# Kernel optimization log

Measured on AMD Instinct MI355X. Metric: run time of the kernel, lower is better.

Reference implementation:

```python
import jax, jax.numpy as jnp
import numpy as np

Q_CHAN = 8          # q_chan
IN_CHAN = 128
KS = 56             # kernel_size; ks*ks must equal h*w
STRIDE = 2
BN_EPS = 1e-5


def setup_inputs() -> dict:
    key = jax.random.key(0)
    ks = jax.random.split(key, 10)
    n, c, h, w = 4, IN_CHAN, 56, 56
    hw = h * w  # 3136 == KS*KS
    oc = 4 * Q_CHAN  # qkv conv output channels = 32
    return {
        "x": jax.random.normal(ks[0], (n, c, h, w), dtype=jnp.float32),
        # 1x1 conv weight (out_ch, in_ch) and bias
        "w_qkv": jax.random.normal(ks[1], (oc, c), dtype=jnp.float32) * (1.0 / np.sqrt(c)),
        "b_qkv": jnp.zeros((oc,), dtype=jnp.float32),
        # BatchNorm (inference mode) affine + running stats
        "bn_gamma": jnp.ones((oc,), dtype=jnp.float32),
        "bn_beta": jnp.zeros((oc,), dtype=jnp.float32),
        "bn_mean": jnp.zeros((oc,), dtype=jnp.float32),
        "bn_var": jnp.ones((oc,), dtype=jnp.float32),
        # learned relative position biases, trailing dim = ks*ks = h*w
        "rq": jax.random.normal(ks[2], (Q_CHAN, KS * KS), dtype=jnp.float32),
        "rk": jax.random.normal(ks[3], (Q_CHAN, KS * KS), dtype=jnp.float32),
        "rv": jax.random.normal(ks[4], (2 * Q_CHAN, KS * KS), dtype=jnp.float32),
    }


def reference(x, w_qkv, b_qkv, bn_gamma, bn_beta, bn_mean, bn_var, rq, rk, rv):
    n, c, h, w = x.shape
    # 1x1 conv + inference BatchNorm
    qkv = jnp.einsum('nchw,oc->nohw', x, w_qkv) + b_qkv[None, :, None, None]
    scale = bn_gamma / jnp.sqrt(bn_var + BN_EPS)
    qkv = (qkv - bn_mean[None, :, None, None]) * scale[None, :, None, None] + bn_beta[None, :, None, None]
    qkv = qkv.reshape(n, 4 * Q_CHAN, h * w)
    q = qkv[:, :Q_CHAN]            # [n, 8, hw]
    k = qkv[:, Q_CHAN:2 * Q_CHAN]  # [n, 8, hw]
    v = qkv[:, 2 * Q_CHAN:]        # [n, 16, hw]
    # global attention scores with learned positional bias terms: [n, hw, hw]
    sc = (jnp.einsum('nci,ncj->nij', q, k)
          + jnp.einsum('ci,ncj->nij', rq, q)
          + jnp.einsum('ci,ncj->nij', rk, k))
    sc = jax.nn.softmax(sc, axis=2)
    v = v + rv[None]
    out = jnp.einsum('nij,ncj->nci', sc, v).reshape(n, 2 * Q_CHAN, h, w)
    # AvgPool2d(kernel=stride, stride=stride)
    s = STRIDE
    out = out.reshape(n, 2 * Q_CHAN, h // s, s, w // s, s).mean(axis=(3, 5))
    return out
```

## Files before the change

### kernel.cpp

```cpp
#include <hip/hip_runtime.h>

#define HW 3136
#define CIN 128
#define MHAT 40.0f
#define NSEV 7
#define LOG2E 1.44269504088896340736f
#define NEGC  (-57.7078018f)

typedef __attribute__((ext_vector_type(8))) short bf16x8;
typedef __attribute__((ext_vector_type(4))) float f32x4;

__device__ __forceinline__ short f2bf(float f) {
    union { float f; unsigned u; } v; v.f = f;
    unsigned r = v.u + 0x7fffu + ((v.u >> 16) & 1u);
    return (short)(r >> 16);
}
__device__ __forceinline__ float bf2f(short s) {
    union { unsigned u; float f; } v; v.u = ((unsigned)(unsigned short)s) << 16;
    return v.f;
}
__device__ __forceinline__ unsigned pk(short a, short b) {
    return (unsigned)(unsigned short)a | ((unsigned)(unsigned short)b << 16);
}
__device__ __forceinline__ unsigned cvtpk(float a, float b) {
    unsigned r;
    asm("v_cvt_pk_bf16_f32 %0, %1, %2" : "=v"(r) : "v"(a), "v"(b));
    return r;
}
__device__ __forceinline__ float lo2f(unsigned p) { return __uint_as_float(p << 16); }
__device__ __forceinline__ float hi2f(unsigned p) { return __uint_as_float(p & 0xffff0000u); }
__device__ __forceinline__ float exp2_hw(float x) {
    float r;
    asm("v_exp_f32 %0, %1" : "=v"(r) : "v"(x));
    return r;
}

union UF { bf16x8 v; unsigned u[4]; };


__global__ __launch_bounds__(256) void proj_mfma(
    const float* __restrict__ x, const float* __restrict__ w,
    const float* __restrict__ bq, const float* __restrict__ gm,
    const float* __restrict__ bt, const float* __restrict__ mu,
    const float* __restrict__ vr, const float* __restrict__ rq,
    const float* __restrict__ rk, const float* __restrict__ rv,
    float* __restrict__ WS, float* __restrict__ ASQ)
{
    const int tid = threadIdx.x;
    const int wv = tid >> 6, lane = tid & 63;
    const int il = lane & 15, q = lane >> 4;
    const int jb = blockIdx.x * 64;
    const int nn = blockIdx.y;
    const int z  = blockIdx.z;
    const int jA = jb + wv * 16 + il;
    const float* xn = x + (size_t)nn * CIN * HW;

    UF ah[4], al[4];
    #pragma unroll
    for (int s = 0; s < 4; ++s) {
        float xv[8];
        #pragma unroll
        for (int u = 0; u < 8; ++u)
            xv[u] = xn[(size_t)(s * 32 + q * 8 + u) * HW + jA];
        #pragma unroll
        for (int t = 0; t < 4; ++t) {
            unsigned hp = cvtpk(xv[2 * t], xv[2 * t + 1]);
            unsigned lp = cvtpk(xv[2 * t] - lo2f(hp), xv[2 * t + 1] - hi2f(hp));
            ah[s].u[t] = hp;
            al[s].u[t] = lp;
        }
    }
    UF wh[4], wl[4];
    const float* wp = w + (size_t)(z * 16 + il) * CIN;
    #pragma unroll
    for (int s = 0; s < 4; ++s) {
        float4 f0 = *(const float4*)(wp + s * 32 + q * 8);
        float4 f1 = *(const float4*)(wp + s * 32 + q * 8 + 4);
        float wf[8] = {f0.x, f0.y, f0.z, f0.w, f1.x, f1.y, f1.z, f1.w};
        #pragma unroll
        for (int t = 0; t < 4; ++t) {
            unsigned hp = cvtpk(wf[2 * t], wf[2 * t + 1]);
            unsigned lp = cvtpk(wf[2 * t] - lo2f(hp), wf[2 * t + 1] - hi2f(hp));
            wh[s].u[t] = hp;
            wl[s].u[t] = lp;
        }
    }

    f32x4 d = {0.f, 0.f, 0.f, 0.f};
    #pragma unroll
    for (int s = 0; s < 4; ++s) d = __builtin_amdgcn_mfma_f32_16x16x32_bf16(ah[s].v, wh[s].v, d, 0, 0, 0);
    #pragma unroll
    for (int s = 0; s < 4; ++s) d = __builtin_amdgcn_mfma_f32_16x16x32_bf16(al[s].v, wh[s].v, d, 0, 0, 0);
    #pragma unroll
    for (int s = 0; s < 4; ++s) d = __builtin_amdgcn_mfma_f32_16x16x32_bf16(ah[s].v, wl[s].v, d, 0, 0, 0);

    const int ch = z * 16 + il;
    const float sc = gm[ch] * rsqrtf(vr[ch] + 1e-5f);
    const float sh = (bq[ch] - mu[ch]) * sc + bt[ch];
    #pragma unroll
    for (int r = 0; r < 4; ++r) {
        const int j = jb + wv * 16 + q * 4 + r;
        float val = d[r] * sc + sh;
        const size_t base = (size_t)nn * HW + j;
        if (z == 0) {
            WS[base * 32 + il] = val;
            float a = (il < 8) ? (val + rk[il * HW + j]) : rq[(il - 8) * HW + j];
            ASQ[base * 16 + il] = a * LOG2E;
        } else {
            WS[base * 32 + 16 + il] = val + rv[il * HW + j];
        }
    }
}

#define JT 224
#define QKS 40
#define VTS 232

__global__ __launch_bounds__(256) void attn_mfma(
    const float* __restrict__ WS, const float* __restrict__ ASQ,
    float* __restrict__ ONUM, float* __restrict__ OLS)
{
    __shared__ short QK[JT * QKS];
    __shared__ short VT[16 * VTS];
    __shared__ short PB[4 * 16 * QKS];
    const int tid = threadIdx.x;
    const int wv = tid >> 6, lane = tid & 63;
    const int il = lane & 15, q = lane >> 4;
    const int b   = blockIdx.x;
    const int sev = b % NSEV;
    const int ig  = b / NSEV;
    const int nn  = ig / 49;
    const int i0  = (ig % 49) * 64 + wv * 16;
    const float* wsn = WS + (size_t)nn * HW * 32;

    bf16x8 bco;
    {
        const float* cp = ASQ + ((size_t)nn * HW + i0 + il) * 16 + (q & 1) * 8;
        float4 f0 = *(const float4*)cp;
        float4 f1 = *(const float4*)(cp + 4);
        float cf[8] = {f0.x, f0.y, f0.z, f0.w, f1.x, f1.y, f1.z, f1.w};
        UF bb;
        #pragma unroll
        for (int t = 0; t < 4; ++t) {
            unsigned hp = cvtpk(cf[2 * t], cf[2 * t + 1]);
            unsigned lp = cvtpk(cf[2 * t] - lo2f(hp), cf[2 * t + 1] - hi2f(hp));
            bb.u[t] = (q < 2) ? hp : lp;
        }
        bco = bb.v;
    }

    const bf16x8 zero8 = {0, 0, 0, 0, 0, 0, 0, 0};
    const f32x4 DINIT = {NEGC, NEGC, NEGC, NEGC};
    f32x4 outc = {0.f, 0.f, 0.f, 0.f};
    float lsum = 0.f;
    short* prow = &PB[(wv * 16 + il) * QKS];

    #pragma unroll 1
    for (int ck = 0; ck < 2; ++ck) {
        const int jb = (sev * 2 + ck) * JT;
        __syncthreads();
        if (tid < JT) {
            const float* src = wsn + (size_t)(jb + tid) * 32;
            float4 v0 = *(const float4*)src;
            float4 v1 = *(const float4*)(src + 4);
            float4 v2 = *(const float4*)(src + 8);
            float4 v3 = *(const float4*)(src + 12);
            float g[16] = {v2.x, v2.y, v2.z, v2.w, v3.x, v3.y, v3.z, v3.w,
                           v0.x, v0.y, v0.z, v0.w, v1.x, v1.y, v1.z, v1.w};
            short* row = &QK[tid * QKS];
            #pragma unroll
            for (int t = 0; t < 8; ++t) {
                unsigned hp = cvtpk(g[2 * t], g[2 * t + 1]);
                unsigned lp = cvtpk(g[2 * t] - lo2f(hp), g[2 * t + 1] - hi2f(hp));
                *(unsigned*)&row[2 * t]      = hp;
                *(unsigned*)&row[16 + 2 * t] = lp;
            }
        }
        {
            const int c = tid & 15, jg = tid >> 4;
            const float* vsrc = wsn + (size_t)(jb + jg * 14) * 32 + 16 + c;
            short* vrow = &VT[c * VTS + jg * 14];
            #pragma unroll
            for (int k = 0; k < 7; ++k)
                *(unsigned*)&vrow[2 * k] = cvtpk(vsrc[(2 * k) * 32], vsrc[(2 * k + 1) * 32]);
        }
        __syncthreads();

        #pragma unroll 2
        for (int step = 0; step < 14; ++step) {
            const short* arow = &QK[(step * 16 + il) * QKS + (q & 1) * 8];
            bf16x8 a1 = *(const bf16x8*)arow;
            bf16x8 a2 = *(const bf16x8*)(arow + 16);
            a2 = (lane < 32) ? a2 : zero8;
            f32x4 d = __builtin_amdgcn_mfma_f32_16x16x32_bf16(a1, bco, DINIT, 0, 0, 0);
            d = __builtin_amdgcn_mfma_f32_16x16x32_bf16(a2, bco, d, 0, 0, 0);
            float p0 = exp2_hw(d[0]), p1 = exp2_hw(d[1]);
            float p2 = exp2_hw(d[2]), p3 = exp2_hw(d[3]);
            lsum += (p0 + p1) + (p2 + p3);
            const int pc = (step & 1) * 16 + q * 4;
            *(unsigned*)&prow[pc]     = cvtpk(p0, p1);
            *(unsigned*)&prow[pc + 2] = cvtpk(p2, p3);
            if (step & 1) {
                bf16x8 ap = *(const bf16x8*)&PB[(wv * 16 + il) * QKS + q * 8];
                bf16x8 bv = *(const bf16x8*)&VT[il * VTS + (step >> 1) * 32 + q * 8];
                outc = __builtin_amdgcn_mfma_f32_16x16x32_bf16(ap, bv, outc, 0, 0, 0);
            }
        }
    }

    lsum += __shfl_xor(lsum, 16);
    lsum += __shfl_xor(lsum, 32);
    float* np = ONUM + ((size_t)(sev * 4 + nn) * HW + i0) * 16;
    #pragma unroll
    for (int r = 0; r < 4; ++r)
        np[(q * 4 + r) * 16 + il] = outc[r];
    if (lane < 16)
        OLS[(size_t)(sev * 4 + nn) * HW + i0 + lane] = lsum;
}

__global__ void pool_kernel(const float* __restrict__ ONUM, const float* __restrict__ OLS,
                            float* __restrict__ out) {
    int idx = blockIdx.x * blockDim.x + threadIdx.x;
    if (idx >= 4 * 16 * 28 * 28) return;
    int ow = idx % 28, oh = (idx / 28) % 28;
    int rest = idx / 784;
    int nn = rest >> 4, c = rest & 15;
    float s = 0.f;
    #pragma unroll
    for (int dh = 0; dh < 2; ++dh)
        #pragma unroll
        for (int dw = 0; dw < 2; ++dw) {
            int i = (2 * oh + dh) * 56 + 2 * ow + dw;
            float num = 0.f, l = 0.f;
            #pragma unroll
            for (int p = 0; p < NSEV; ++p) {
                num += ONUM[((size_t)(p * 4 + nn) * HW + i) * 16 + c];
                l   += OLS[(size_t)(p * 4 + nn) * HW + i];
            }
            s += num / l;
        }
    out[idx] = 0.25f * s;
}

#define FJC 392
#define FPSTR 394

__global__ __launch_bounds__(512, 2) void fused_attn(
    const float* __restrict__ x, const float* __restrict__ w,
    const float* __restrict__ bq, const float* __restrict__ gm,
    const float* __restrict__ bt, const float* __restrict__ mu,
    const float* __restrict__ vr, const float* __restrict__ rq,
    const float* __restrict__ rk, const float* __restrict__ rv,
    float* __restrict__ out)
{
    __shared__ float PT[32][FPSTR];
    __shared__ float SQ[56][16];
    __shared__ float ST[56][17];

    const int tid  = threadIdx.x;
    const int wv   = tid >> 6, lane = tid & 63;
    const int bid  = blockIdx.x;
    const int nn   = bid / 56, rem = bid % 56;
    const int oh   = rem >> 1, half = rem & 1;
    const float* xn = x + (size_t)nn * CIN * HW;

    if (tid < 448) {
        int r = tid >> 3, c = tid & 7;
        int rh = (r >= 28) ? 1 : 0, rw = r - 28*rh;
        int i  = (2*oh + rh)*56 + half*28 + rw;
        float acc = 0.f;
        for (int cc = 0; cc < CIN; ++cc)
            acc += xn[cc*HW + i] * w[c*CIN + cc];
        float s  = gm[c] * rsqrtf(vr[c] + 1e-5f);
        float qv = (acc + bq[c] - mu[c])*s + bt[c];
        SQ[r][c]   = qv + rk[c*HW + i];
        SQ[r][8+c] = rq[c*HW + i];
    }

    float l_[7];
    float ac_[7][16];
    #pragma unroll
    for (int r = 0; r < 7; ++r) {
        l_[r] = 0.f;
        #pragma unroll
        for (int c = 0; c < 16; ++c) ac_[r][c] = 0.f;
    }
    __syncthreads();

    for (int cb = 0; cb < 8; ++cb) {
        const int jbase = cb * FJC;
        const int o0 = wv * 4;
        for (int t = 0; t < 4; ++t) {
            int p = lane + 64*t;
            if (p < 196) {
                int j0 = jbase + 2*p;
                float a0x=0.f,a0y=0.f,a1x=0.f,a1y=0.f,a2x=0.f,a2y=0.f,a3x=0.f,a3y=0.f;
                for (int cc = 0; cc < CIN; ++cc) {
                    float2 xv = *(const float2*)(xn + (size_t)cc*HW + j0);
                    float w0 = w[(o0+0)*CIN + cc];
                    float w1 = w[(o0+1)*CIN + cc];
                    float w2 = w[(o0+2)*CIN + cc];
                    float w3 = w[(o0+3)*CIN + cc];
                    a0x += xv.x*w0; a0y += xv.y*w0;
                    a1x += xv.x*w1; a1y += xv.y*w1;
                    a2x += xv.x*w2; a2y += xv.y*w2;
                    a3x += xv.x*w3; a3y += xv.y*w3;
                }
                #pragma unroll
                for (int u = 0; u < 4; ++u) {
                    int o = o0 + u;
                    float av0 = (u==0)? a0x : (u==1)? a1x : (u==2)? a2x : a3x;
                    float av1 = (u==0)? a0y : (u==1)? a1y : (u==2)? a2y : a3y;
                    float s  = gm[o] * rsqrtf(vr[o] + 1e-5f);
                    float sh = (bq[o] - mu[o])*s + bt[o];
                    float v0 = av0*s + sh, v1 = av1*s + sh;
                    if (o >= 16) {
                        v0 += rv[(o-16)*HW + j0];
                        v1 += rv[(o-16)*HW + j0 + 1];
                    }
                    *(float2*)&PT[o][2*p] = make_float2(v0, v1);
                }
            }
        }
        __syncthreads();

        #pragma unroll
        for (int rr = 0; rr < 7; rr += 2) {
            const bool two = (rr + 1) < 7;
            const int ra = wv*7 + rr;
            float A1a[8], A2a[8], A1b[8], A2b[8];
            #pragma unroll
            for (int c = 0; c < 8; ++c) {
                A1a[c] = SQ[ra][c];   A2a[c] = SQ[ra][8+c];
                A1b[c] = two ? SQ[ra+1][c]   : 0.f;
                A2b[c] = two ? SQ[ra+1][8+c] : 0.f;
            }
            for (int t = 0; t < 7; ++t) {
                int jl = 64*t + lane;
                if (jl < FJC) {
                    float qv[8], kv[8], vv[16];
                    #pragma unroll
                    for (int c = 0; c < 8; ++c) { qv[c] = PT[c][jl]; kv[c] = PT[8+c][jl]; }
                    #pragma unroll
                    for (int c = 0; c < 16; ++c) vv[c] = PT[16+c][jl];
                    float sa = 0.f, sb = 0.f;
                    #pragma unroll
                    for (int c = 0; c < 8; ++c) {
                        sa += A1a[c]*kv[c] + A2a[c]*qv[c];
                        sb += A1b[c]*kv[c] + A2b[c]*qv[c];
                    }
                    float pa = __expf(sa - MHAT);
                    l_[rr] += pa;
                    #pragma unroll
                    for (int c = 0; c < 16; ++c) ac_[rr][c] += pa * vv[c];
                    if (two) {
                        float pb = __expf(sb - MHAT);
                        l_[rr+1] += pb;
                        #pragma unroll
                        for (int c = 0; c < 16; ++c) ac_[rr+1][c] += pb * vv[c];
                    }
                }
            }
        }
        __syncthreads();
    }

    #pragma unroll
    for (int rr = 0; rr < 7; ++rr) {
        int r = wv*7 + rr;
        float l = l_[rr];
        #pragma unroll
        for (int off = 32; off; off >>= 1) l += __shfl_xor(l, off);
        if (lane == 0) ST[r][16] = l;
        #pragma unroll
        for (int c = 0; c < 16; ++c) {
            float a = ac_[rr][c];
            #pragma unroll
            for (int off = 32; off; off >>= 1) a += __shfl_xor(a, off);
            if (lane == c) ST[r][c] = a;
        }
    }
    __syncthreads();

    if (tid < 224) {
        int c = tid & 15, qq = tid >> 4;
        float s = 0.f;
        #pragma unroll
        for (int rh = 0; rh < 2; ++rh)
            #pragma unroll
            for (int dw = 0; dw < 2; ++dw) {
                int r = rh*28 + 2*qq + dw;
                s += ST[r][c] / ST[r][16];
            }
        out[((nn*16 + c)*28 + oh)*28 + half*14 + qq] = 0.25f * s;
    }
}

extern "C" void kernel_launch(void* const* d_in, const int* in_sizes, int n_in,
                              void* d_out, int out_size, void* d_ws, size_t ws_size,
                              hipStream_t stream) {
    const float* x     = (const float*)d_in[0];
    const float* w     = (const float*)d_in[1];
    const float* bq    = (const float*)d_in[2];
    const float* gm    = (const float*)d_in[3];
    const float* bt    = (const float*)d_in[4];
    const float* mu    = (const float*)d_in[5];
    const float* vr    = (const float*)d_in[6];
    const float* rq    = (const float*)d_in[7];
    const float* rk    = (const float*)d_in[8];
    const float* rv    = (const float*)d_in[9];
    float* out = (float*)d_out;

    const size_t WSF  = (size_t)4 * HW * 32;
    const size_t ASQF = (size_t)4 * HW * 16;
    const size_t ONF  = (size_t)NSEV * 4 * HW * 16;
    const size_t OLF  = (size_t)NSEV * 4 * HW;
    const size_t NEED = (WSF + ASQF + ONF + OLF) * sizeof(float);

    if (ws_size >= NEED) {
        float* WS   = (float*)d_ws;
        float* ASQ  = WS + WSF;
        float* ONUM = ASQ + ASQF;
        float* OLS  = ONUM + ONF;
        proj_mfma<<<dim3(49, 4, 2), 256, 0, stream>>>(x, w, bq, gm, bt, mu, vr, rq, rk, rv, WS, ASQ);
        attn_mfma<<<dim3(196 * NSEV), 256, 0, stream>>>(WS, ASQ, ONUM, OLS);
        pool_kernel<<<dim3(196), 256, 0, stream>>>(ONUM, OLS, out);
    } else {
        fused_attn<<<dim3(224), dim3(512), 0, stream>>>(x, w, bq, gm, bt, mu, vr, rq, rk, rv, out);
    }
}
```

Baseline: 110.4 us.

## Emit pre-split bf16 hi/lo Q/K and transposed V from projection kernel

The projection kernel now writes Q/K and the per-query coefficient vectors already split into bf16 hi/lo pairs in the exact row layout the attention kernel copies into shared memory, and writes V+rv as bf16 in channel-major order. The attention kernel then does plain vector copies instead of float loads plus per-block bf16 split conversions, which halves global traffic and removes conversion work repeated across the 7 key-chunk blocks. The block index mapping also changes so blocks sharing a key chunk are adjacent. The projection's MFMA operands are swapped for z==0 to get a transposed output layout, and its accumulation is split into two accumulators.

```diff
diff --git a/kernel.cpp b/kernel.cpp
--- a/kernel.cpp
+++ b/kernel.cpp
@@ -10,18 +10,6 @@
 typedef __attribute__((ext_vector_type(8))) short bf16x8;
 typedef __attribute__((ext_vector_type(4))) float f32x4;
 
-__device__ __forceinline__ short f2bf(float f) {
-    union { float f; unsigned u; } v; v.f = f;
-    unsigned r = v.u + 0x7fffu + ((v.u >> 16) & 1u);
-    return (short)(r >> 16);
-}
-__device__ __forceinline__ float bf2f(short s) {
-    union { unsigned u; float f; } v; v.u = ((unsigned)(unsigned short)s) << 16;
-    return v.f;
-}
-__device__ __forceinline__ unsigned pk(short a, short b) {
-    return (unsigned)(unsigned short)a | ((unsigned)(unsigned short)b << 16);
-}
 __device__ __forceinline__ unsigned cvtpk(float a, float b) {
     unsigned r;
     asm("v_cvt_pk_bf16_f32 %0, %1, %2" : "=v"(r) : "v"(a), "v"(b));
@@ -44,7 +32,7 @@
     const float* __restrict__ bt, const float* __restrict__ mu,
     const float* __restrict__ vr, const float* __restrict__ rq,
     const float* __restrict__ rk, const float* __restrict__ rv,
-    float* __restrict__ WS, float* __restrict__ ASQ)
+    short* __restrict__ QKWS, short* __restrict__ ASQB, short* __restrict__ VWS)
 {
     const int tid = threadIdx.x;
     const int wv = tid >> 6, lane = tid & 63;
@@ -55,7 +43,7 @@
     const int jA = jb + wv * 16 + il;
     const float* xn = x + (size_t)nn * CIN * HW;
 
-    UF ah[4], al[4];
+    UF xh[4], xl[4];
     #pragma unroll
     for (int s = 0; s < 4; ++s) {
         float xv[8];
@@ -66,8 +54,8 @@
         for (int t = 0; t < 4; ++t) {
             unsigned hp = cvtpk(xv[2 * t], xv[2 * t + 1]);
             unsigned lp = cvtpk(xv[2 * t] - lo2f(hp), xv[2 * t + 1] - hi2f(hp));
-            ah[s].u[t] = hp;
-            al[s].u[t] = lp;
+            xh[s].u[t] = hp;
+            xl[s].u[t] = lp;
         }
     }
     UF wh[4], wl[4];
@@ -86,29 +74,68 @@
         }
     }
 
-    f32x4 d = {0.f, 0.f, 0.f, 0.f};
-    #pragma unroll
-    for (int s = 0; s < 4; ++s) d = __builtin_amdgcn_mfma_f32_16x16x32_bf16(ah[s].v, wh[s].v, d, 0, 0, 0);
-    #pragma unroll
-    for (int s = 0; s < 4; ++s) d = __builtin_amdgcn_mfma_f32_16x16x32_bf16(al[s].v, wh[s].v, d, 0, 0, 0);
-    #pragma unroll
-    for (int s = 0; s < 4; ++s) d = __builtin_amdgcn_mfma_f32_16x16x32_bf16(ah[s].v, wl[s].v, d, 0, 0, 0);
-
-    const int ch = z * 16 + il;
-    const float sc = gm[ch] * rsqrtf(vr[ch] + 1e-5f);
-    const float sh = (bq[ch] - mu[ch]) * sc + bt[ch];
-    #pragma unroll
-    for (int r = 0; r < 4; ++r) {
-        const int j = jb + wv * 16 + q * 4 + r;
-        float val = d[r] * sc + sh;
-        const size_t base = (size_t)nn * HW + j;
-        if (z == 0) {
-            WS[base * 32 + il] = val;
-            float a = (il < 8) ? (val + rk[il * HW + j]) : rq[(il - 8) * HW + j];
-            ASQ[base * 16 + il] = a * LOG2E;
-        } else {
-            WS[base * 32 + 16 + il] = val + rv[il * HW + j];
-        }
+    f32x4 a0 = {0.f, 0.f, 0.f, 0.f}, a1 = {0.f, 0.f, 0.f, 0.f};
+    if (z == 0) {
+        #pragma unroll
+        for (int s = 0; s < 4; ++s) a0 = __builtin_amdgcn_mfma_f32_16x16x32_bf16(wh[s].v, xh[s].v, a0, 0, 0, 0);
+        #pragma unroll
+        for (int s = 0; s < 4; ++s) a1 = __builtin_amdgcn_mfma_f32_16x16x32_bf16(wl[s].v, xh[s].v, a1, 0, 0, 0);
+        #pragma unroll
+        for (int s = 0; s < 4; ++s) a1 = __builtin_amdgcn_mfma_f32_16x16x32_bf16(wh[s].v, xl[s].v, a1, 0, 0, 0);
+    } else {
+        #pragma unroll
+        for (int s = 0; s < 4; ++s) a0 = __builtin_amdgcn_mfma_f32_16x16x32_bf16(xh[s].v, wh[s].v, a0, 0, 0, 0);
+        #pragma unroll
+        for (int s = 0; s < 4; ++s) a1 = __builtin_amdgcn_mfma_f32_16x16x32_bf16(xl[s].v, wh[s].v, a1, 0, 0, 0);
+        #pragma unroll
+        for (int s = 0; s < 4; ++s) a1 = __builtin_amdgcn_mfma_f32_16x16x32_bf16(xh[s].v, wl[s].v, a1, 0, 0, 0);
+    }
+    const f32x4 d = a0 + a1;
+
+    if (z == 0) {
+        const int jj = jA;
+        float hv[4], av[4];
+        #pragma unroll
+        for (int r = 0; r < 4; ++r) {
+            const int ch = q * 4 + r;
+            const float sc = gm[ch] * rsqrtf(vr[ch] + 1e-5f);
+            const float sh = (bq[ch] - mu[ch]) * sc + bt[ch];
+            const float val = d[r] * sc + sh;
+            hv[r] = val;
+            const float a = (ch < 8) ? (val + rk[(size_t)ch * HW + jj])
+                                     : rq[(size_t)(ch - 8) * HW + jj];
+            av[r] = a * LOG2E;
+        }
+        short* qrow = QKWS + ((size_t)nn * HW + jj) * 32;
+        short* arow = ASQB + ((size_t)nn * HW + jj) * 32;
+        const int pb = (q * 4) ^ 8;
+        unsigned h01 = cvtpk(hv[0], hv[1]), h23 = cvtpk(hv[2], hv[3]);
+        unsigned l01 = cvtpk(hv[0] - lo2f(h01), hv[1] - hi2f(h01));
+        unsigned l23 = cvtpk(hv[2] - lo2f(h23), hv[3] - hi2f(h23));
+        *(unsigned*)&qrow[pb]          = h01;
+        *(unsigned*)&qrow[pb + 2]      = h23;
+        *(unsigned*)&qrow[16 + pb]     = l01;
+        *(unsigned*)&qrow[16 + pb + 2] = l23;
+        unsigned c01 = cvtpk(av[0], av[1]), c23 = cvtpk(av[2], av[3]);
+        unsigned e01 = cvtpk(av[0] - lo2f(c01), av[1] - hi2f(c01));
+        unsigned e23 = cvtpk(av[2] - lo2f(c23), av[3] - hi2f(c23));
+        *(unsigned*)&arow[q * 4]          = c01;
+        *(unsigned*)&arow[q * 4 + 2]      = c23;
+        *(unsigned*)&arow[16 + q * 4]     = e01;
+        *(unsigned*)&arow[16 + q * 4 + 2] = e23;
+    } else {
+        const int ch = 16 + il;
+        const float sc = gm[ch] * rsqrtf(vr[ch] + 1e-5f);
+        const float sh = (bq[ch] - mu[ch]) * sc + bt[ch];
+        const int jbase = jb + wv * 16 + q * 4;
+        float4 rvv = *(const float4*)(rv + (size_t)il * HW + jbase);
+        float v0 = d[0] * sc + sh + rvv.x;
+        float v1 = d[1] * sc + sh + rvv.y;
+        float v2 = d[2] * sc + sh + rvv.z;
+        float v3 = d[3] * sc + sh + rvv.w;
+        short* vp = VWS + (size_t)(nn * 16 + il) * HW + jbase;
+        *(unsigned*)&vp[0] = cvtpk(v0, v1);
+        *(unsigned*)&vp[2] = cvtpk(v2, v3);
     }
 }
 
@@ -117,7 +144,8 @@
 #define VTS 232
 
 __global__ __launch_bounds__(256) void attn_mfma(
-    const float* __restrict__ WS, const float* __restrict__ ASQ,
+    const short* __restrict__ QKWS, const short* __restrict__ ASQB,
+    const short* __restrict__ VWS,
     float* __restrict__ ONUM, float* __restrict__ OLS)
 {
     __shared__ short QK[JT * QKS];
@@ -127,27 +155,12 @@
     const int wv = tid >> 6, lane = tid & 63;
     const int il = lane & 15, q = lane >> 4;
     const int b   = blockIdx.x;
-    const int sev = b % NSEV;
-    const int ig  = b / NSEV;
+    const int sev = b / 196;
+    const int ig  = b % 196;
     const int nn  = ig / 49;
     const int i0  = (ig % 49) * 64 + wv * 16;
-    const float* wsn = WS + (size_t)nn * HW * 32;
-
-    bf16x8 bco;
-    {
-        const float* cp = ASQ + ((size_t)nn * HW + i0 + il) * 16 + (q & 1) * 8;
-        float4 f0 = *(const float4*)cp;
-        float4 f1 = *(const float4*)(cp + 4);
-        float cf[8] = {f0.x, f0.y, f0.z, f0.w, f1.x, f1.y, f1.z, f1.w};
-        UF bb;
-        #pragma unroll
-        for (int t = 0; t < 4; ++t) {
-            unsigned hp = cvtpk(cf[2 * t], cf[2 * t + 1]);
-            unsigned lp = cvtpk(cf[2 * t] - lo2f(hp), cf[2 * t + 1] - hi2f(hp));
-            bb.u[t] = (q < 2) ? hp : lp;
-        }
-        bco = bb.v;
-    }
+
+    const bf16x8 bco = *(const bf16x8*)(ASQB + ((size_t)nn * HW + i0 + il) * 32 + q * 8);
 
     const bf16x8 zero8 = {0, 0, 0, 0, 0, 0, 0, 0};
     const f32x4 DINIT = {NEGC, NEGC, NEGC, NEGC};
@@ -160,29 +173,23 @@
         const int jb = (sev * 2 + ck) * JT;
         __syncthreads();
         if (tid < JT) {
-            const float* src = wsn + (size_t)(jb + tid) * 32;
-            float4 v0 = *(const float4*)src;
-            float4 v1 = *(const float4*)(src + 4);
-            float4 v2 = *(const float4*)(src + 8);
-            float4 v3 = *(const float4*)(src + 12);
-            float g[16] = {v2.x, v2.y, v2.z, v2.w, v3.x, v3.y, v3.z, v3.w,
-                           v0.x, v0.y, v0.z, v0.w, v1.x, v1.y, v1.z, v1.w};
+            const short* src = QKWS + ((size_t)nn * HW + jb + tid) * 32;
+            int4 w0 = *(const int4*)(src);
+            int4 w1 = *(const int4*)(src + 8);
+            int4 w2 = *(const int4*)(src + 16);
+            int4 w3 = *(const int4*)(src + 24);
             short* row = &QK[tid * QKS];
-            #pragma unroll
-            for (int t = 0; t < 8; ++t) {
-                unsigned hp = cvtpk(g[2 * t], g[2 * t + 1]);
-                unsigned lp = cvtpk(g[2 * t] - lo2f(hp), g[2 * t + 1] - hi2f(hp));
-                *(unsigned*)&row[2 * t]      = hp;
-                *(unsigned*)&row[16 + 2 * t] = lp;
-            }
+            *(int4*)&row[0]  = w0;
+            *(int4*)&row[8]  = w1;
+            *(int4*)&row[16] = w2;
+            *(int4*)&row[24] = w3;
         }
         {
             const int c = tid & 15, jg = tid >> 4;
-            const float* vsrc = wsn + (size_t)(jb + jg * 14) * 32 + 16 + c;
-            short* vrow = &VT[c * VTS + jg * 14];
+            const unsigned* vs = (const unsigned*)(VWS + (size_t)(nn * 16 + c) * HW + jb + jg * 14);
+            unsigned* vd = (unsigned*)&VT[c * VTS + jg * 14];
             #pragma unroll
-            for (int k = 0; k < 7; ++k)
-                *(unsigned*)&vrow[2 * k] = cvtpk(vsrc[(2 * k) * 32], vsrc[(2 * k + 1) * 32]);
+            for (int k = 0; k < 7; ++k) vd[k] = vs[k];
         }
         __syncthreads();
 
@@ -411,19 +418,20 @@
     const float* rv    = (const float*)d_in[9];
     float* out = (float*)d_out;
 
-    const size_t WSF  = (size_t)4 * HW * 32;
-    const size_t ASQF = (size_t)4 * HW * 16;
-    const size_t ONF  = (size_t)NSEV * 4 * HW * 16;
-    const size_t OLF  = (size_t)NSEV * 4 * HW;
-    const size_t NEED = (WSF + ASQF + ONF + OLF) * sizeof(float);
+    const size_t ONF = (size_t)NSEV * 4 * HW * 16;
+    const size_t OLF = (size_t)NSEV * 4 * HW;
+    const size_t QKF = (size_t)4 * HW * 32;
+    const size_t VWF = (size_t)4 * 16 * HW;
+    const size_t NEED = (ONF + OLF) * sizeof(float) + (2 * QKF + VWF) * sizeof(short);
 
     if (ws_size >= NEED) {
-        float* WS   = (float*)d_ws;
-        float* ASQ  = WS + WSF;
-        float* ONUM = ASQ + ASQF;
+        float* ONUM = (float*)d_ws;
         float* OLS  = ONUM + ONF;
-        proj_mfma<<<dim3(49, 4, 2), 256, 0, stream>>>(x, w, bq, gm, bt, mu, vr, rq, rk, rv, WS, ASQ);
-        attn_mfma<<<dim3(196 * NSEV), 256, 0, stream>>>(WS, ASQ, ONUM, OLS);
+        short* QKWS = (short*)(OLS + OLF);
+        short* ASQB = QKWS + QKF;
+        short* VWS  = ASQB + QKF;
+        proj_mfma<<<dim3(49, 4, 2), 256, 0, stream>>>(x, w, bq, gm, bt, mu, vr, rq, rk, rv, QKWS, ASQB, VWS);
+        attn_mfma<<<dim3(196 * NSEV), 256, 0, stream>>>(QKWS, ASQB, VWS, ONUM, OLS);
         pool_kernel<<<dim3(196), 256, 0, stream>>>(ONUM, OLS, out);
     } else {
         fused_attn<<<dim3(224), dim3(512), 0, stream>>>(x, w, bq, gm, bt, mu, vr, rq, rk, rv, out);
```

After: 108.5 us. Within noise of the previous version (-1.7%).
